# Optimization experiments

Measured on AMD Instinct MI355X. Metric: run time of the kernel, lower is better.

Reference implementation:

```python
import jax, jax.numpy as jnp
import numpy as np

INPUT_DIM = 784
LATENT_DIM = 32
HIDDEN = 256
NUM_PROTO = 25  # 5x5 SOM grid
BATCH = 65536


def setup_inputs() -> dict:
    key = jax.random.key(0)
    ks = jax.random.split(key, 10)
    s = lambda fan_in: 1.0 / np.sqrt(fan_in)
    return {
        "x": jax.random.uniform(ks[0], (BATCH, INPUT_DIM), dtype=jnp.float32),
        # encoder: Linear(784,256) -> ReLU -> Linear(256,32)
        "We1": jax.random.normal(ks[1], (INPUT_DIM, HIDDEN), dtype=jnp.float32) * s(INPUT_DIM),
        "be1": jnp.zeros((HIDDEN,), dtype=jnp.float32),
        "We2": jax.random.normal(ks[2], (HIDDEN, LATENT_DIM), dtype=jnp.float32) * s(HIDDEN),
        "be2": jnp.zeros((LATENT_DIM,), dtype=jnp.float32),
        # decoder: Linear(32,256) -> ReLU -> Linear(256,784) -> Sigmoid
        "Wd1": jax.random.normal(ks[3], (LATENT_DIM, HIDDEN), dtype=jnp.float32) * s(LATENT_DIM),
        "bd1": jnp.zeros((HIDDEN,), dtype=jnp.float32),
        "Wd2": jax.random.normal(ks[4], (HIDDEN, INPUT_DIM), dtype=jnp.float32) * s(HIDDEN),
        "bd2": jnp.zeros((INPUT_DIM,), dtype=jnp.float32),
        # SOM prototypes (torch.randn init)
        "prototypes": jax.random.normal(ks[5], (NUM_PROTO, LATENT_DIM), dtype=jnp.float32),
    }


def reference(x, We1, be1, We2, be2, Wd1, bd1, Wd2, bd2, prototypes):
    # encoder
    h = jax.nn.relu(x @ We1 + be1)          # [B, 256]
    z = h @ We2 + be2                        # [B, 32]
    # SOM layer: cdist -> argmin -> gather winning prototype
    # squared euclidean distance suffices for argmin
    sq_dists = (jnp.sum(z * z, axis=1, keepdims=True)
                - 2.0 * (z @ prototypes.T)
                + jnp.sum(prototypes * prototypes, axis=1))  # [B, 25]
    min_idx = jnp.argmin(sq_dists, axis=1)   # [B]
    som_z = prototypes[min_idx]              # [B, 32]
    # decoder
    hd = jax.nn.relu(som_z @ Wd1 + bd1)      # [B, 256]
    x_recon = jax.nn.sigmoid(hd @ Wd2 + bd2)  # [B, 784]
    return (x_recon, z, som_z)
```

## Files before the change

kernel.cpp:

```cpp
#include <hip/hip_runtime.h>
#include <hip/hip_bf16.h>
#include <math.h>

#define BATCH   65536
#define IN_DIM  784
#define HID     256
#define LAT     32
#define NPROTO  25

typedef short  short8  __attribute__((ext_vector_type(8)));
typedef float  floatx4 __attribute__((ext_vector_type(4)));

__device__ __forceinline__ unsigned short f2bf(float v) {
    __hip_bfloat16 b = __float2bfloat16(v);
    return *reinterpret_cast<unsigned short*>(&b);
}
__device__ __forceinline__ float bf2f(unsigned short u) {
    __hip_bfloat16 b = *reinterpret_cast<__hip_bfloat16*>(&u);
    return __bfloat162float(b);
}
__device__ __forceinline__ void split3(float v, unsigned short& o1,
                                       unsigned short& o2, unsigned short& o3) {
    o1 = f2bf(v); float r1 = v - bf2f(o1);
    o2 = f2bf(r1); float r2 = r1 - bf2f(o2);
    o3 = f2bf(r2);
}

__device__ __forceinline__ floatx4 mm_bf16(short8 a, short8 b, floatx4 c) {
    return __builtin_amdgcn_mfma_f32_16x16x32_bf16(a, b, c, 0, 0, 0);
}

__device__ __forceinline__ void async_copy16(const void* g, void* l) {
    __builtin_amdgcn_global_load_lds(
        (const __attribute__((address_space(1))) unsigned int*)g,
        (__attribute__((address_space(3))) unsigned int*)l, 16, 0, 0);
}

#define BT_BYTES   409600
#define WS_NEEDED  1307200

__global__ __launch_bounds__(256)
void prep_B(const float* __restrict__ We1,
            unsigned short* __restrict__ B1,
            unsigned short* __restrict__ B2,
            unsigned short* __restrict__ B3)
{
    int e = (blockIdx.x * 256 + threadIdx.x) * 4;
    int k = e & 31;
    int n = (e >> 5) & 255;
    int s = e >> 13;
    int cs = (k >> 3) ^ ((n >> 1) & 3);
    int dst = (s * 256 + n) * 32 + cs * 8 + (k & 7);
    ushort4 u1, u2, u3;
    unsigned short a, b, c;
#pragma unroll
    for (int j = 0; j < 4; ++j) {
        int kk = s * 32 + k + j;
        float v = (kk < IN_DIM) ? We1[(size_t)kk * HID + n] : 0.f;
        split3(v, a, b, c);
        ((unsigned short*)&u1)[j] = a;
        ((unsigned short*)&u2)[j] = b;
        ((unsigned short*)&u3)[j] = c;
    }
    *(ushort4*)(B1 + dst) = u1;
    *(ushort4*)(B2 + dst) = u2;
    *(ushort4*)(B3 + dst) = u3;
}

__global__ __launch_bounds__(256)
void dpsom_dectab(const float* __restrict__ protos,
                  const float* __restrict__ Wd1,
                  const float* __restrict__ bd1,
                  const float* __restrict__ Wd2,
                  const float* __restrict__ bd2,
                  float* __restrict__ table)
{
    __shared__ float pr[LAT];
    __shared__ float hd[HID];
    const int p = blockIdx.x;
    const int tid = threadIdx.x;
    if (tid < LAT) pr[tid] = protos[p * LAT + tid];
    __syncthreads();
    float s = bd1[tid];
#pragma unroll
    for (int k = 0; k < LAT; ++k)
        s = fmaf(pr[k], Wd1[k * HID + tid], s);
    hd[tid] = fmaxf(s, 0.f);
    __syncthreads();
    for (int i = tid; i < IN_DIM; i += 256) {
        float o = bd2[i];
        for (int j = 0; j < HID; ++j)
            o = fmaf(hd[j], Wd2[(size_t)j * IN_DIM + i], o);
        table[p * IN_DIM + i] = 1.f / (1.f + expf(-o));
    }
}

__global__ __launch_bounds__(256, 2)
void dpsom_encoder_mfma(const float* __restrict__ x,
                        const unsigned short* __restrict__ B1g,
                        const unsigned short* __restrict__ B2g,
                        const unsigned short* __restrict__ B3g,
                        const float* __restrict__ be1,
                        const float* __restrict__ We2,
                        const float* __restrict__ be2,
                        const float* __restrict__ protos,
                        const float* __restrict__ table,
                        float* __restrict__ z_out,
                        float* __restrict__ somz_out,
                        float* __restrict__ xrec)
{
    __shared__ __align__(16) char smem[61440];
    const int tid  = threadIdx.x;
    const int wave = tid >> 6;
    const int lane = tid & 63;
    const int l15  = lane & 15;
    const int q    = lane >> 4;
    const int sw   = (l15 >> 1) & 3;
    const int row0 = blockIdx.x * 64;

    floatx4 acc[4][4];
#pragma unroll
    for (int i = 0; i < 4; ++i)
#pragma unroll
        for (int j = 0; j < 4; ++j) acc[i][j] = (floatx4)0.f;

    for (int s = 0; s < 25; ++s) {
        __syncthreads();
        {
            size_t gbase = (size_t)s * 16384 + (size_t)wave * 4096 + (size_t)lane * 16;
            char* lb = smem + 12288 + wave * 4096 + lane * 16;
#pragma unroll
            for (int i = 0; i < 4; ++i) {
                async_copy16((const char*)B1g + gbase + i * 1024, lb + 0     + i * 1024);
                async_copy16((const char*)B2g + gbase + i * 1024, lb + 16384 + i * 1024);
                async_copy16((const char*)B3g + gbase + i * 1024, lb + 32768 + i * 1024);
            }
        }
#pragma unroll
        for (int i = 0; i < 2; ++i) {
            int ff  = tid + i * 256;
            int row = ff >> 3;
            int k4  = ff & 7;
            float4 v = make_float4(0.f, 0.f, 0.f, 0.f);
            if (s < 24 || k4 < 4)
                v = *(const float4*)(x + (size_t)(row0 + row) * IN_DIM + s * 32 + k4 * 4);
            ushort4 u1, u2, u3;
            unsigned short a, b, c;
            split3(v.x, a, b, c); u1.x = a; u2.x = b; u3.x = c;
            split3(v.y, a, b, c); u1.y = a; u2.y = b; u3.y = c;
            split3(v.z, a, b, c); u1.z = a; u2.z = b; u3.z = c;
            split3(v.w, a, b, c); u1.w = a; u2.w = b; u3.w = c;
            int csw = ((k4 >> 1) ^ ((row >> 1) & 3));
            int dst = row * 64 + csw * 16 + (k4 & 1) * 8;
            *(ushort4*)(smem + dst)        = u1;
            *(ushort4*)(smem + 4096 + dst) = u2;
            *(ushort4*)(smem + 8192 + dst) = u3;
        }
        __syncthreads();

        short8 afr[3][4];
#pragma unroll
        for (int mf = 0; mf < 4; ++mf) {
            int abyte = (16 * mf + l15) * 64 + ((q ^ sw) * 16);
            afr[0][mf] = *(short8*)(smem + abyte);
            afr[1][mf] = *(short8*)(smem + 4096 + abyte);
            afr[2][mf] = *(short8*)(smem + 8192 + abyte);
        }
#pragma unroll
        for (int nf = 0; nf < 4; ++nf) {
            int n = wave * 64 + 16 * nf + l15;
            int bbyte = n * 64 + ((q ^ sw) * 16);
            short8 b1 = *(short8*)(smem + 12288 + bbyte);
            short8 b2 = *(short8*)(smem + 28672 + bbyte);
            short8 b3 = *(short8*)(smem + 45056 + bbyte);
#pragma unroll
            for (int mf = 0; mf < 4; ++mf) {
                floatx4 t = acc[mf][nf];
                t = mm_bf16(afr[0][mf], b1, t);
                t = mm_bf16(afr[0][mf], b2, t);
                t = mm_bf16(afr[1][mf], b1, t);
                t = mm_bf16(afr[1][mf], b2, t);
                t = mm_bf16(afr[0][mf], b3, t);
                t = mm_bf16(afr[2][mf], b1, t);
                acc[mf][nf] = t;
            }
        }
    }

    {
        float bias[4];
#pragma unroll
        for (int nf = 0; nf < 4; ++nf) bias[nf] = be1[wave * 64 + 16 * nf + l15];
#pragma unroll
        for (int mf = 0; mf < 4; ++mf)
#pragma unroll
            for (int nf = 0; nf < 4; ++nf)
#pragma unroll
                for (int r = 0; r < 4; ++r)
                    acc[mf][nf][r] = fmaxf(acc[mf][nf][r] + bias[nf], 0.f);
    }

    float* h_lds = (float*)smem;
    float* z_lds = (float*)(smem + 33280);
    int*  minidx = (int*)(smem + 41728);

    const int jz = tid & 31;
    const int rg = tid >> 5;
    const float bz = be2[jz];

    for (int half = 0; half < 2; ++half) {
        __syncthreads();
#pragma unroll
        for (int mm = 0; mm < 2; ++mm) {
            int mf = 2 * half + mm;
#pragma unroll
            for (int nf = 0; nf < 4; ++nf)
#pragma unroll
                for (int r = 0; r < 4; ++r) {
                    int lr = 16 * mm + 4 * q + r;
                    h_lds[lr * 260 + wave * 64 + 16 * nf + l15] = acc[mf][nf][r];
                }
        }
        __syncthreads();
        float s0 = bz, s1 = bz, s2 = bz, s3 = bz;
        const float* h0p = h_lds + (rg * 4 + 0) * 260;
        const float* h1p = h_lds + (rg * 4 + 1) * 260;
        const float* h2p = h_lds + (rg * 4 + 2) * 260;
        const float* h3p = h_lds + (rg * 4 + 3) * 260;
#pragma unroll 4
        for (int c = 0; c < HID; c += 4) {
            float w0 = We2[(c + 0) * LAT + jz];
            float w1 = We2[(c + 1) * LAT + jz];
            float w2 = We2[(c + 2) * LAT + jz];
            float w3 = We2[(c + 3) * LAT + jz];
            float4 h0 = *(const float4*)(h0p + c);
            float4 h1 = *(const float4*)(h1p + c);
            float4 h2 = *(const float4*)(h2p + c);
            float4 h3 = *(const float4*)(h3p + c);
            s0 = fmaf(h0.x, w0, fmaf(h0.y, w1, fmaf(h0.z, w2, fmaf(h0.w, w3, s0))));
            s1 = fmaf(h1.x, w0, fmaf(h1.y, w1, fmaf(h1.z, w2, fmaf(h1.w, w3, s1))));
            s2 = fmaf(h2.x, w0, fmaf(h2.y, w1, fmaf(h2.z, w2, fmaf(h2.w, w3, s2))));
            s3 = fmaf(h3.x, w0, fmaf(h3.y, w1, fmaf(h3.z, w2, fmaf(h3.w, w3, s3))));
        }
        int rbase = half * 32 + rg * 4;
        z_lds[(rbase + 0) * 33 + jz] = s0;
        z_lds[(rbase + 1) * 33 + jz] = s1;
        z_lds[(rbase + 2) * 33 + jz] = s2;
        z_lds[(rbase + 3) * 33 + jz] = s3;
        z_out[(size_t)(row0 + rbase + 0) * LAT + jz] = s0;
        z_out[(size_t)(row0 + rbase + 1) * LAT + jz] = s1;
        z_out[(size_t)(row0 + rbase + 2) * LAT + jz] = s2;
        z_out[(size_t)(row0 + rbase + 3) * LAT + jz] = s3;
    }
    __syncthreads();

    if (tid < 64) {
        float zr[LAT];
        float zn = 0.f;
#pragma unroll
        for (int j = 0; j < LAT; ++j) {
            zr[j] = z_lds[tid * 33 + j];
            zn = fmaf(zr[j], zr[j], zn);
        }
        float best = 3.4e38f;
        int bp = 0;
        for (int p = 0; p < NPROTO; ++p) {
            float dot = 0.f, pn = 0.f;
#pragma unroll
            for (int j = 0; j < LAT; ++j) {
                float pv = protos[p * LAT + j];
                dot = fmaf(zr[j], pv, dot);
                pn  = fmaf(pv, pv, pn);
            }
            float d = zn - 2.f * dot + pn;
            if (d < best) { best = d; bp = p; }
        }
        minidx[tid] = bp;
    }
    __syncthreads();

#pragma unroll
    for (int m = 0; m < 8; ++m) {
        int r = rg * 8 + m;
        somz_out[(size_t)(row0 + r) * LAT + jz] = protos[minidx[r] * LAT + jz];
    }

    for (int i2 = tid; i2 < 64 * 196; i2 += 256) {
        int row = i2 / 196;
        int c   = i2 - row * 196;
        int idx = minidx[row];
        ((float4*)xrec)[(size_t)(row0 + row) * 196 + c] =
            ((const float4*)table)[idx * 196 + c];
    }
}

#define BMf 64
#define BKf 16
#define HSTRIDE 260
#define ZSTRIDE 33
#define SMEM_FLOATS 10432

__global__ __launch_bounds__(256)
void dpsom_encoder_fp32(const float* __restrict__ x,
                        const float* __restrict__ We1,
                        const float* __restrict__ be1,
                        const float* __restrict__ We2,
                        const float* __restrict__ be2,
                        const float* __restrict__ protos,
                        float* __restrict__ z_out,
                        float* __restrict__ somz_out,
                        int* __restrict__ minidx_out)
{
    __shared__ float smem[SMEM_FLOATS];
    __shared__ int minidx_lds[BMf];
    float* As = smem;
    float* Bs = smem + BKf * BMf;
    float* h_lds = smem;
    float* z_lds = smem + 32 * HSTRIDE;

    const int tid = threadIdx.x;
    const int tx = tid & 31;
    const int ty = tid >> 5;
    const int row0 = blockIdx.x * BMf;

    float acc[8][8];
#pragma unroll
    for (int i = 0; i < 8; ++i)
#pragma unroll
        for (int j = 0; j < 8; ++j) acc[i][j] = 0.f;

    const int ar  = tid >> 2;
    const int akq = tid & 3;

    for (int k0 = 0; k0 < IN_DIM; k0 += BKf) {
        __syncthreads();
        float4 av = *(const float4*)(x + (size_t)(row0 + ar) * IN_DIM + k0 + akq * 4);
        As[(akq * 4 + 0) * BMf + ar] = av.x;
        As[(akq * 4 + 1) * BMf + ar] = av.y;
        As[(akq * 4 + 2) * BMf + ar] = av.z;
        As[(akq * 4 + 3) * BMf + ar] = av.w;
#pragma unroll
        for (int i = 0; i < 4; ++i) {
            int f  = tid + i * 256;
            int bk = f >> 6;
            int bn = (f & 63) << 2;
            *(float4*)(Bs + bk * HID + bn) =
                *(const float4*)(We1 + (size_t)(k0 + bk) * HID + bn);
        }
        __syncthreads();
#pragma unroll
        for (int kk = 0; kk < BKf; ++kk) {
            float4 a0 = *(const float4*)(As + kk * BMf + ty * 8);
            float4 a1 = *(const float4*)(As + kk * BMf + ty * 8 + 4);
            float4 b0 = *(const float4*)(Bs + kk * HID + tx * 8);
            float4 b1 = *(const float4*)(Bs + kk * HID + tx * 8 + 4);
            float a[8] = {a0.x, a0.y, a0.z, a0.w, a1.x, a1.y, a1.z, a1.w};
            float b[8] = {b0.x, b0.y, b0.z, b0.w, b1.x, b1.y, b1.z, b1.w};
#pragma unroll
            for (int i = 0; i < 8; ++i)
#pragma unroll
                for (int j = 0; j < 8; ++j)
                    acc[i][j] = fmaf(a[i], b[j], acc[i][j]);
        }
    }
    {
        float bias[8];
#pragma unroll
        for (int j = 0; j < 8; ++j) bias[j] = be1[tx * 8 + j];
#pragma unroll
        for (int i = 0; i < 8; ++i)
#pragma unroll
            for (int j = 0; j < 8; ++j)
                acc[i][j] = fmaxf(acc[i][j] + bias[j], 0.f);
    }
    const int jz = tid & 31;
    const int rg = tid >> 5;
    const float bz = be2[jz];
    for (int half = 0; half < 2; ++half) {
        __syncthreads();
        if ((ty >> 2) == half) {
            int rb = (ty & 3) * 8;
#pragma unroll
            for (int i = 0; i < 8; ++i) {
                *(float4*)(h_lds + (rb + i) * HSTRIDE + tx * 8) =
                    make_float4(acc[i][0], acc[i][1], acc[i][2], acc[i][3]);
                *(float4*)(h_lds + (rb + i) * HSTRIDE + tx * 8 + 4) =
                    make_float4(acc[i][4], acc[i][5], acc[i][6], acc[i][7]);
            }
        }
        __syncthreads();
        float s0 = bz, s1 = bz, s2 = bz, s3 = bz;
        const float* h0p = h_lds + (rg * 4 + 0) * HSTRIDE;
        const float* h1p = h_lds + (rg * 4 + 1) * HSTRIDE;
        const float* h2p = h_lds + (rg * 4 + 2) * HSTRIDE;
        const float* h3p = h_lds + (rg * 4 + 3) * HSTRIDE;
#pragma unroll 4
        for (int c = 0; c < HID; c += 4) {
            float w0 = We2[(c + 0) * LAT + jz];
            float w1 = We2[(c + 1) * LAT + jz];
            float w2 = We2[(c + 2) * LAT + jz];
            float w3 = We2[(c + 3) * LAT + jz];
            float4 h0 = *(const float4*)(h0p + c);
            float4 h1 = *(const float4*)(h1p + c);
            float4 h2 = *(const float4*)(h2p + c);
            float4 h3 = *(const float4*)(h3p + c);
            s0 = fmaf(h0.x, w0, fmaf(h0.y, w1, fmaf(h0.z, w2, fmaf(h0.w, w3, s0))));
            s1 = fmaf(h1.x, w0, fmaf(h1.y, w1, fmaf(h1.z, w2, fmaf(h1.w, w3, s1))));
            s2 = fmaf(h2.x, w0, fmaf(h2.y, w1, fmaf(h2.z, w2, fmaf(h2.w, w3, s2))));
            s3 = fmaf(h3.x, w0, fmaf(h3.y, w1, fmaf(h3.z, w2, fmaf(h3.w, w3, s3))));
        }
        int rbase = half * 32 + rg * 4;
        z_lds[(rbase + 0) * ZSTRIDE + jz] = s0;
        z_lds[(rbase + 1) * ZSTRIDE + jz] = s1;
        z_lds[(rbase + 2) * ZSTRIDE + jz] = s2;
        z_lds[(rbase + 3) * ZSTRIDE + jz] = s3;
        z_out[(size_t)(row0 + rbase + 0) * LAT + jz] = s0;
        z_out[(size_t)(row0 + rbase + 1) * LAT + jz] = s1;
        z_out[(size_t)(row0 + rbase + 2) * LAT + jz] = s2;
        z_out[(size_t)(row0 + rbase + 3) * LAT + jz] = s3;
    }
    __syncthreads();
    if (tid < BMf) {
        float zr[LAT];
        float zn = 0.f;
#pragma unroll
        for (int j = 0; j < LAT; ++j) {
            zr[j] = z_lds[tid * ZSTRIDE + j];
            zn = fmaf(zr[j], zr[j], zn);
        }
        float best = 3.4e38f;
        int bp = 0;
        for (int p = 0; p < NPROTO; ++p) {
            float dot = 0.f, pn = 0.f;
#pragma unroll
            for (int j = 0; j < LAT; ++j) {
                float pv = protos[p * LAT + j];
                dot = fmaf(zr[j], pv, dot);
                pn  = fmaf(pv, pv, pn);
            }
            float d = zn - 2.f * dot + pn;
            if (d < best) { best = d; bp = p; }
        }
        minidx_out[row0 + tid] = bp;
        minidx_lds[tid] = bp;
    }
    __syncthreads();
#pragma unroll
    for (int m = 0; m < 8; ++m) {
        int r = rg * 8 + m;
        somz_out[(size_t)(row0 + r) * LAT + jz] = protos[minidx_lds[r] * LAT + jz];
    }
}

__global__ __launch_bounds__(256)
void dpsom_gather(const float4* __restrict__ table,
                  const int* __restrict__ minidx,
                  float4* __restrict__ xrec)
{
    const int f = blockIdx.x * 256 + threadIdx.x;
    const int row = f / 196;
    const int c4  = f - row * 196;
    const int idx = minidx[row];
    xrec[f] = table[idx * 196 + c4];
}

extern "C" void kernel_launch(void* const* d_in, const int* in_sizes, int n_in,
                              void* d_out, int out_size, void* d_ws, size_t ws_size,
                              hipStream_t stream)
{
    const float* x    = (const float*)d_in[0];
    const float* We1  = (const float*)d_in[1];
    const float* be1  = (const float*)d_in[2];
    const float* We2  = (const float*)d_in[3];
    const float* be2  = (const float*)d_in[4];
    const float* Wd1  = (const float*)d_in[5];
    const float* bd1  = (const float*)d_in[6];
    const float* Wd2  = (const float*)d_in[7];
    const float* bd2  = (const float*)d_in[8];
    const float* prot = (const float*)d_in[9];

    float* out   = (float*)d_out;
    float* xrec  = out;
    float* z_out = out + (size_t)BATCH * IN_DIM;
    float* somz  = z_out + (size_t)BATCH * LAT;

    if (ws_size >= WS_NEEDED) {
        unsigned short* B1 = (unsigned short*)d_ws;
        unsigned short* B2 = (unsigned short*)((char*)d_ws + BT_BYTES);
        unsigned short* B3 = (unsigned short*)((char*)d_ws + 2 * BT_BYTES);
        float* table = (float*)((char*)d_ws + 3 * BT_BYTES);

        hipLaunchKernelGGL(prep_B, dim3(200), dim3(256), 0, stream, We1, B1, B2, B3);
        hipLaunchKernelGGL(dpsom_dectab, dim3(NPROTO), dim3(256), 0, stream,
                           prot, Wd1, bd1, Wd2, bd2, table);
        hipLaunchKernelGGL(dpsom_encoder_mfma, dim3(BATCH / 64), dim3(256), 0, stream,
                           x, B1, B2, B3, be1, We2, be2, prot, table,
                           z_out, somz, xrec);
    } else {
        int*   minidx = (int*)d_ws;
        float* table  = (float*)((char*)d_ws + (size_t)BATCH * 4);
        hipLaunchKernelGGL(dpsom_encoder_fp32, dim3(BATCH / BMf), dim3(256), 0, stream,
                           x, We1, be1, We2, be2, prot, z_out, somz, minidx);
        hipLaunchKernelGGL(dpsom_dectab, dim3(NPROTO), dim3(256), 0, stream,
                           prot, Wd1, bd1, Wd2, bd2, table);
        hipLaunchKernelGGL(dpsom_gather, dim3((BATCH * (IN_DIM / 4)) / 256), dim3(256), 0, stream,
                           (const float4*)table, minidx, (float4*)xrec);
    }
}
```

Measured before the change: 512.3 us.

## Merge prep kernels into one launch and register-prefetch next x tile

Combines the weight-splitting prep kernel and the decoder-table kernel into a single launch that picks its role by block index, removing one launch and letting the two jobs run concurrently. In the encoder main loop, the x slice for the next K-step is loaded into registers before the current step's split and MFMA work, so global load latency overlaps compute. Per-thread address and swizzle offsets are also hoisted out of the loop. The prefetch costs extra registers, which could pressure the 2-blocks-per-SM occupancy target.

```diff
diff --git a/kernel.cpp b/kernel.cpp
--- a/kernel.cpp
+++ b/kernel.cpp
@@ -40,58 +40,57 @@
 #define WS_NEEDED  1307200
 
 __global__ __launch_bounds__(256)
-void prep_B(const float* __restrict__ We1,
-            unsigned short* __restrict__ B1,
-            unsigned short* __restrict__ B2,
-            unsigned short* __restrict__ B3)
+void dpsom_prep(const float* __restrict__ We1,
+                unsigned short* __restrict__ B1,
+                unsigned short* __restrict__ B2,
+                unsigned short* __restrict__ B3,
+                const float* __restrict__ protos,
+                const float* __restrict__ Wd1,
+                const float* __restrict__ bd1,
+                const float* __restrict__ Wd2,
+                const float* __restrict__ bd2,
+                float* __restrict__ table)
 {
-    int e = (blockIdx.x * 256 + threadIdx.x) * 4;
-    int k = e & 31;
-    int n = (e >> 5) & 255;
-    int s = e >> 13;
-    int cs = (k >> 3) ^ ((n >> 1) & 3);
-    int dst = (s * 256 + n) * 32 + cs * 8 + (k & 7);
-    ushort4 u1, u2, u3;
-    unsigned short a, b, c;
-#pragma unroll
-    for (int j = 0; j < 4; ++j) {
-        int kk = s * 32 + k + j;
-        float v = (kk < IN_DIM) ? We1[(size_t)kk * HID + n] : 0.f;
-        split3(v, a, b, c);
-        ((unsigned short*)&u1)[j] = a;
-        ((unsigned short*)&u2)[j] = b;
-        ((unsigned short*)&u3)[j] = c;
-    }
-    *(ushort4*)(B1 + dst) = u1;
-    *(ushort4*)(B2 + dst) = u2;
-    *(ushort4*)(B3 + dst) = u3;
-}
-
-__global__ __launch_bounds__(256)
-void dpsom_dectab(const float* __restrict__ protos,
-                  const float* __restrict__ Wd1,
-                  const float* __restrict__ bd1,
-                  const float* __restrict__ Wd2,
-                  const float* __restrict__ bd2,
-                  float* __restrict__ table)
-{
-    __shared__ float pr[LAT];
-    __shared__ float hd[HID];
-    const int p = blockIdx.x;
     const int tid = threadIdx.x;
-    if (tid < LAT) pr[tid] = protos[p * LAT + tid];
-    __syncthreads();
-    float s = bd1[tid];
-#pragma unroll
-    for (int k = 0; k < LAT; ++k)
-        s = fmaf(pr[k], Wd1[k * HID + tid], s);
-    hd[tid] = fmaxf(s, 0.f);
-    __syncthreads();
-    for (int i = tid; i < IN_DIM; i += 256) {
-        float o = bd2[i];
-        for (int j = 0; j < HID; ++j)
-            o = fmaf(hd[j], Wd2[(size_t)j * IN_DIM + i], o);
-        table[p * IN_DIM + i] = 1.f / (1.f + expf(-o));
+    if (blockIdx.x < 200) {
+        int e = (blockIdx.x * 256 + tid) * 4;
+        int k = e & 31;
+        int n = (e >> 5) & 255;
+        int s = e >> 13;
+        int cs = (k >> 3) ^ ((n >> 1) & 3);
+        int dst = (s * 256 + n) * 32 + cs * 8 + (k & 7);
+        ushort4 u1, u2, u3;
+        unsigned short a, b, c;
+#pragma unroll
+        for (int j = 0; j < 4; ++j) {
+            int kk = s * 32 + k + j;
+            float v = (kk < IN_DIM) ? We1[(size_t)kk * HID + n] : 0.f;
+            split3(v, a, b, c);
+            ((unsigned short*)&u1)[j] = a;
+            ((unsigned short*)&u2)[j] = b;
+            ((unsigned short*)&u3)[j] = c;
+        }
+        *(ushort4*)(B1 + dst) = u1;
+        *(ushort4*)(B2 + dst) = u2;
+        *(ushort4*)(B3 + dst) = u3;
+    } else {
+        __shared__ float pr[LAT];
+        __shared__ float hd[HID];
+        const int p = blockIdx.x - 200;
+        if (tid < LAT) pr[tid] = protos[p * LAT + tid];
+        __syncthreads();
+        float s = bd1[tid];
+#pragma unroll
+        for (int k = 0; k < LAT; ++k)
+            s = fmaf(pr[k], Wd1[k * HID + tid], s);
+        hd[tid] = fmaxf(s, 0.f);
+        __syncthreads();
+        for (int i = tid; i < IN_DIM; i += 256) {
+            float o = bd2[i];
+            for (int j = 0; j < HID; ++j)
+                o = fmaf(hd[j], Wd2[(size_t)j * IN_DIM + i], o);
+            table[p * IN_DIM + i] = 1.f / (1.f + expf(-o));
+        }
     }
 }
 
@@ -124,8 +123,32 @@
 #pragma unroll
         for (int j = 0; j < 4; ++j) acc[i][j] = (floatx4)0.f;
 
+    int row_[2], k4_[2], dst_[2];
+    const float* xptr[2];
+#pragma unroll
+    for (int i = 0; i < 2; ++i) {
+        int ff = tid + i * 256;
+        row_[i] = ff >> 3;
+        k4_[i]  = ff & 7;
+        int csw = ((k4_[i] >> 1) ^ ((row_[i] >> 1) & 3));
+        dst_[i] = row_[i] * 64 + csw * 16 + (k4_[i] & 1) * 8;
+        xptr[i] = x + (size_t)(row0 + row_[i]) * IN_DIM + k4_[i] * 4;
+    }
+
+    float4 cur[2], nxt[2];
+#pragma unroll
+    for (int i = 0; i < 2; ++i) cur[i] = *(const float4*)(xptr[i]);
+
     for (int s = 0; s < 25; ++s) {
         __syncthreads();
+        if (s < 24) {
+#pragma unroll
+            for (int i = 0; i < 2; ++i) {
+                nxt[i] = make_float4(0.f, 0.f, 0.f, 0.f);
+                if (s + 1 < 24 || k4_[i] < 4)
+                    nxt[i] = *(const float4*)(xptr[i] + (s + 1) * 32);
+            }
+        }
         {
             size_t gbase = (size_t)s * 16384 + (size_t)wave * 4096 + (size_t)lane * 16;
             char* lb = smem + 12288 + wave * 4096 + lane * 16;
@@ -138,23 +161,16 @@
         }
 #pragma unroll
         for (int i = 0; i < 2; ++i) {
-            int ff  = tid + i * 256;
-            int row = ff >> 3;
-            int k4  = ff & 7;
-            float4 v = make_float4(0.f, 0.f, 0.f, 0.f);
-            if (s < 24 || k4 < 4)
-                v = *(const float4*)(x + (size_t)(row0 + row) * IN_DIM + s * 32 + k4 * 4);
+            float4 v = cur[i];
             ushort4 u1, u2, u3;
             unsigned short a, b, c;
             split3(v.x, a, b, c); u1.x = a; u2.x = b; u3.x = c;
             split3(v.y, a, b, c); u1.y = a; u2.y = b; u3.y = c;
             split3(v.z, a, b, c); u1.z = a; u2.z = b; u3.z = c;
             split3(v.w, a, b, c); u1.w = a; u2.w = b; u3.w = c;
-            int csw = ((k4 >> 1) ^ ((row >> 1) & 3));
-            int dst = row * 64 + csw * 16 + (k4 & 1) * 8;
-            *(ushort4*)(smem + dst)        = u1;
-            *(ushort4*)(smem + 4096 + dst) = u2;
-            *(ushort4*)(smem + 8192 + dst) = u3;
+            *(ushort4*)(smem + dst_[i])        = u1;
+            *(ushort4*)(smem + 4096 + dst_[i]) = u2;
+            *(ushort4*)(smem + 8192 + dst_[i]) = u3;
         }
         __syncthreads();
 
@@ -185,6 +201,8 @@
                 acc[mf][nf] = t;
             }
         }
+#pragma unroll
+        for (int i = 0; i < 2; ++i) cur[i] = nxt[i];
     }
 
     {
@@ -453,6 +471,34 @@
 }
 
 __global__ __launch_bounds__(256)
+void dpsom_dectab(const float* __restrict__ protos,
+                  const float* __restrict__ Wd1,
+                  const float* __restrict__ bd1,
+                  const float* __restrict__ Wd2,
+                  const float* __restrict__ bd2,
+                  float* __restrict__ table)
+{
+    __shared__ float pr[LAT];
+    __shared__ float hd[HID];
+    const int p = blockIdx.x;
+    const int tid = threadIdx.x;
+    if (tid < LAT) pr[tid] = protos[p * LAT + tid];
+    __syncthreads();
+    float s = bd1[tid];
+#pragma unroll
+    for (int k = 0; k < LAT; ++k)
+        s = fmaf(pr[k], Wd1[k * HID + tid], s);
+    hd[tid] = fmaxf(s, 0.f);
+    __syncthreads();
+    for (int i = tid; i < IN_DIM; i += 256) {
+        float o = bd2[i];
+        for (int j = 0; j < HID; ++j)
+            o = fmaf(hd[j], Wd2[(size_t)j * IN_DIM + i], o);
+        table[p * IN_DIM + i] = 1.f / (1.f + expf(-o));
+    }
+}
+
+__global__ __launch_bounds__(256)
 void dpsom_gather(const float4* __restrict__ table,
                   const int* __restrict__ minidx,
                   float4* __restrict__ xrec)
@@ -490,9 +536,8 @@
         unsigned short* B3 = (unsigned short*)((char*)d_ws + 2 * BT_BYTES);
         float* table = (float*)((char*)d_ws + 3 * BT_BYTES);
 
-        hipLaunchKernelGGL(prep_B, dim3(200), dim3(256), 0, stream, We1, B1, B2, B3);
-        hipLaunchKernelGGL(dpsom_dectab, dim3(NPROTO), dim3(256), 0, stream,
-                           prot, Wd1, bd1, Wd2, bd2, table);
+        hipLaunchKernelGGL(dpsom_prep, dim3(225), dim3(256), 0, stream,
+                           We1, B1, B2, B3, prot, Wd1, bd1, Wd2, bd2, table);
         hipLaunchKernelGGL(dpsom_encoder_mfma, dim3(BATCH / 64), dim3(256), 0, stream,
                            x, B1, B2, B3, be1, We2, be2, prot, table,
                            z_out, somz, xrec);
```

New measurement: 547.4 us. 1.07x slower.
